# Optimization experiments

Hardware: AMD Instinct MI355X
Metric: run time of the kernel (lower is better)

The kernel has to match this reference:

```python
import jax, jax.numpy as jnp
import numpy as np
from jax import lax

B, C, H, W = 4, 256, 32, 32   # latent: NCHW, C == codebook embed dim
N_CODES = 16384


def setup_inputs() -> dict:
    key = jax.random.key(0)
    k1, k2, k3 = jax.random.split(key, 3)
    latent = jax.random.normal(k1, (B, C, H, W), jnp.float32)
    codebook = jax.random.normal(k2, (N_CODES, C), jnp.float32)
    dec_w = jax.random.normal(k3, (3, C, 3, 3), jnp.float32) * 0.02
    dec_b = jnp.zeros((3,), jnp.float32)
    return {"latent": latent, "codebook": codebook, "dec_w": dec_w, "dec_b": dec_b}


def vector_quantize(x, codebook):
    # x: [B,H,W,D], codebook: [N,D]. Squared-L2 nearest neighbor + gather,
    # straight-through gradient (replace_grad(x_q, x)).
    d = ((x * x).sum(-1, keepdims=True)
         - 2.0 * jnp.einsum('bhwd,nd->bhwn', x, codebook)
         + (codebook * codebook).sum(-1))          # [B,H,W,N]
    idx = jnp.argmin(d, axis=-1)                    # [B,H,W]
    x_q = codebook[idx]                             # gather -> [B,H,W,D]
    return x + lax.stop_gradient(x_q - x)


@jax.custom_vjp
def clamp_with_grad(x):
    return jnp.clip(x, 0.0, 1.0)

def _cwg_fwd(x):
    return jnp.clip(x, 0.0, 1.0), x

def _cwg_bwd(x, g):
    # pass gradient only where it points back toward the valid range
    keep = (g * (x - jnp.clip(x, 0.0, 1.0)) >= 0).astype(g.dtype)
    return (g * keep,)

clamp_with_grad.defvjp(_cwg_fwd, _cwg_bwd)


def decode(quant, dec_w, dec_b):
    # stub VQGAN decoder: single 3x3 conv embed_dim -> 3 (NCHW)
    y = lax.conv_general_dilated(quant, dec_w, window_strides=(1, 1),
                                 padding='SAME',
                                 dimension_numbers=('NCHW', 'OIHW', 'NCHW'))
    return y + dec_b[None, :, None, None]


def reference(latent, codebook, dec_w, dec_b):
    x = jnp.moveaxis(latent, 1, 3)                  # NCHW -> NHWC
    quant = jnp.moveaxis(vector_quantize(x, codebook), 3, 1)  # back to NCHW
    img = decode(quant, dec_w, dec_b)
    return clamp_with_grad((img + 1.0) * 0.5)
```

## Files before the change

### kernel.cpp

```cpp
#include <hip/hip_runtime.h>
#include <hip/hip_bf16.h>
#include <stdint.h>

#define P_TOT   4096
#define N_CODE  16384
#define DIM     256
#define HW      1024
#define CHW     262144
#define NBLK    16

typedef unsigned long long u64;
typedef unsigned short u16;
typedef __attribute__((ext_vector_type(4))) float f32x4;
typedef __attribute__((ext_vector_type(8))) short bf16x8;
typedef __attribute__((ext_vector_type(8))) unsigned short ushort8;

#define FENCE() asm volatile("" ::: "memory")
#define BAR()   __builtin_amdgcn_s_barrier()
#define VM(n)   asm volatile("s_waitcnt vmcnt(" #n ")" ::: "memory")

__device__ __forceinline__ unsigned int mono(float f) {
  unsigned int u = __float_as_uint(f);
  return (u & 0x80000000u) ? ~u : (u | 0x80000000u);
}
__device__ __forceinline__ u16 f2bf(float f) {
  __hip_bfloat16 h = __float2bfloat16(f);
  return *(u16*)&h;
}
__device__ __forceinline__ float bf2f(u16 b) {
  __hip_bfloat16 h = *(__hip_bfloat16*)&b;
  return __bfloat162float(h);
}
__device__ __forceinline__ void gload16(const void* g, void* l) {
  __builtin_amdgcn_global_load_lds(
      (const __attribute__((address_space(1))) unsigned int*)g,
      (__attribute__((address_space(3))) unsigned int*)l, 16, 0, 0);
}

__global__ __launch_bounds__(256) void k_prep(const float* __restrict__ cb,
                                              const float* __restrict__ latent,
                                              const float* __restrict__ dec_w,
                                              u16* __restrict__ bfrag,
                                              u16* __restrict__ xfrag,
                                              float* __restrict__ xt,
                                              float* __restrict__ cnorm,
                                              float* __restrict__ wt) {
  __shared__ float ls[64][68];
  int bid = blockIdx.x;
  int t = threadIdx.x;
  if (bid < 1024) {
    int blk = bid;
    int kp = blk & 3, bq = (blk >> 2) & 3, nb = blk >> 4;
    int code0 = nb * 256 + bq * 64;
    int k0 = kp * 64;
    int lr = t >> 4, lc = (t & 15) * 4;
    #pragma unroll
    for (int pss = 0; pss < 4; ++pss) {
      int row = pss * 16 + lr;
      float4 v = *(const float4*)&cb[(size_t)(code0 + row) * DIM + k0 + lc];
      ls[row][lc] = v.x; ls[row][lc + 1] = v.y; ls[row][lc + 2] = v.z; ls[row][lc + 3] = v.w;
    }
    __syncthreads();
    int row64 = t & 63, g = t >> 6;
    #pragma unroll
    for (int it = 0; it < 4; ++it) {
      int combo = it * 4 + g;
      int kt2 = combo >> 3, s = (combo >> 1) & 3, h = combo & 1;
      int kt = kp * 2 + kt2;
      ushort8 o;
      #pragma unroll
      for (int e = 0; e < 8; ++e) {
        float x = ls[row64][kt2 * 32 + s * 8 + e];
        u16 hi = f2bf(x);
        o[e] = h ? f2bf(x - bf2f(hi)) : hi;
      }
      size_t unitIdx = (size_t)(nb * 8 + kt) * 4 + bq;
      *(ushort8*)&bfrag[unitIdx * 4096 + (size_t)((h * 4 + s) * 64 + row64) * 8] = o;
    }
  } else if (bid < 1280) {
    int blk = bid - 1024;
    int kp = blk & 3, rowblk = blk >> 2;
    int g0 = rowblk * 64;
    int b = g0 >> 10, hw0 = g0 & 1023;
    int c0 = kp * 64;
    int ch = t >> 4, px4 = (t & 15) * 4;
    #pragma unroll
    for (int pss = 0; pss < 4; ++pss) {
      int c = pss * 16 + ch;
      float4 v = *(const float4*)&latent[(size_t)b * CHW + (size_t)(c0 + c) * HW + hw0 + px4];
      ls[px4 + 0][c] = v.x; ls[px4 + 1][c] = v.y; ls[px4 + 2][c] = v.z; ls[px4 + 3][c] = v.w;
    }
    __syncthreads();
    int row64 = t & 63, g = t >> 6;
    #pragma unroll
    for (int it = 0; it < 4; ++it) {
      int combo = it * 4 + g;
      int kt2 = combo >> 3, s = (combo >> 1) & 3, h = combo & 1;
      int kt = kp * 2 + kt2;
      ushort8 o;
      #pragma unroll
      for (int e = 0; e < 8; ++e) {
        float x = ls[row64][kt2 * 32 + s * 8 + e];
        u16 hi = f2bf(x);
        o[e] = h ? f2bf(x - bf2f(hi)) : hi;
      }
      int mbO = rowblk >> 2, aq = rowblk & 3;
      size_t unitIdx = (size_t)(mbO * 8 + kt) * 4 + aq;
      *(ushort8*)&xfrag[unitIdx * 4096 + (size_t)((h * 4 + s) * 64 + row64) * 8] = o;
    }
    int pix = t >> 2, sub = t & 3;
    #pragma unroll
    for (int q = 0; q < 4; ++q) {
      int c = sub * 16 + q * 4;
      float4 v;
      v.x = ls[pix][c]; v.y = ls[pix][c + 1]; v.z = ls[pix][c + 2]; v.w = ls[pix][c + 3];
      *(float4*)&xt[(size_t)(g0 + pix) * DIM + c0 + c] = v;
    }
  } else if (bid < 5376) {
    int code = (bid - 1280) * 4 + (t >> 6);
    int lane = t & 63;
    float4 v = ((const float4*)(cb + (size_t)code * DIM))[lane];
    float sv = fmaf(v.x, v.x, fmaf(v.y, v.y, fmaf(v.z, v.z, v.w * v.w)));
    #pragma unroll
    for (int off = 32; off; off >>= 1) sv += __shfl_down(sv, off, 64);
    if (lane == 0) cnorm[code] = sv;
  } else {
    int e = (bid - 5376) * 256 + t;
    if (e < 6912) {
      int ic = e & 255; int r = e >> 8;
      int kx = r % 3; r /= 3; int ky = r % 3; int oc = r / 3;
      wt[e] = dec_w[((oc * 256 + ic) * 3 + ky) * 3 + kx];
    }
  }
}

__global__ __launch_bounds__(512, 2) void k_vq(const u16* __restrict__ xfrag,
                                               const u16* __restrict__ bfrag,
                                               const float* __restrict__ cnorm,
                                               u64* __restrict__ partial) {
  __shared__ u16 lds[2][2][4][4096];
  __shared__ float cnl[1024];
  __shared__ u64 red[256][4];

  int bid = blockIdx.x;
  int xcd = bid & 7, ix = bid >> 3;
  int nbc = xcd * 2 + (ix >> 4);
  int mb  = ix & 15;

  int tid = threadIdx.x, lane = tid & 63, w = tid >> 6;
  int fr = lane & 15, s = lane >> 4;
  int wr = w >> 2, wc = w & 3;
  int tid8 = tid * 8;

  const u16* Xb = xfrag + (size_t)mb * 32 * 4096;
  const u16* Bb = bfrag + (size_t)nbc * 128 * 4096;

  cnl[tid]       = cnorm[nbc * 1024 + tid];
  cnl[tid + 512] = cnorm[nbc * 1024 + 512 + tid];
  ((u64*)red)[tid]       = ~0ull;
  ((u64*)red)[tid + 512] = ~0ull;
  __syncthreads();

  #pragma unroll
  for (int r = 0; r < 4; ++r) gload16(Xb + (size_t)r * 4096 + tid8, &lds[0][0][r][0] + tid8);
  #pragma unroll
  for (int r = 0; r < 4; ++r) gload16(Bb + (size_t)r * 4096 + tid8, &lds[0][1][r][0] + tid8);
  VM(0); BAR(); FENCE();

  f32x4 acc[8][4] = {};

  #define FOLD(pp) {                                                          \
    float cnv[4]; unsigned codev[4];                                          \
    _Pragma("unroll")                                                         \
    for (int nf = 0; nf < 4; ++nf) {                                          \
      cnv[nf] = cnl[(pp) * 256 + wc * 64 + nf * 16 + fr];                     \
      codev[nf] = (unsigned)(nbc * 1024 + (pp) * 256 + wc * 64 + nf * 16 + fr); \
    }                                                                         \
    _Pragma("unroll")                                                         \
    for (int mfr = 0; mfr < 8; ++mfr) {                                       \
      u64 bb[4];                                                              \
      _Pragma("unroll")                                                       \
      for (int rr = 0; rr < 4; ++rr) {                                        \
        u64 m = ~0ull;                                                        \
        _Pragma("unroll")                                                     \
        for (int nf = 0; nf < 4; ++nf) {                                      \
          float val = fmaf(-2.0f, acc[mfr][nf][rr], cnv[nf]);                 \
          u64 key = ((u64)mono(val) << 32) | codev[nf];                       \
          if (key < m) m = key;                                               \
        }                                                                     \
        bb[rr] = m;                                                           \
      }                                                                       \
      _Pragma("unroll")                                                       \
      for (int d = 1; d < 16; d <<= 1) {                                      \
        _Pragma("unroll")                                                     \
        for (int rr = 0; rr < 4; ++rr) {                                      \
          u64 o = __shfl_xor(bb[rr], d, 64);                                  \
          if (o < bb[rr]) bb[rr] = o;                                         \
        }                                                                     \
      }                                                                       \
      if (fr == 0) {                                                          \
        _Pragma("unroll")                                                     \
        for (int rr = 0; rr < 4; ++rr) {                                      \
          int row = wr * 128 + mfr * 16 + s * 4 + rr;                         \
          u64 old = red[row][wc];                                             \
          red[row][wc] = (bb[rr] < old) ? bb[rr] : old;                       \
        }                                                                     \
      }                                                                       \
      _Pragma("unroll")                                                       \
      for (int nf = 0; nf < 4; ++nf)                                          \
        _Pragma("unroll")                                                     \
        for (int rr = 0; rr < 4; ++rr) acc[mfr][nf][rr] = 0.0f;               \
    }                                                                         \
  }

  #pragma unroll 1
  for (int tt = 0; tt < 32; ++tt) {
    const int cur = tt & 1, nxt = cur ^ 1;
    const int kt = tt & 7;
    const u16* LA = &lds[cur][0][0][0];
    const u16* LB = &lds[cur][1][0][0];
    if (tt < 31) {
      const u16* SA = Xb + (size_t)((tt + 1) & 7) * 16384;
      const u16* SB = Bb + (size_t)(tt + 1) * 16384;
      #pragma unroll
      for (int r = 0; r < 4; ++r) gload16(SA + (size_t)r * 4096 + tid8, &lds[nxt][0][r][0] + tid8);
      #pragma unroll
      for (int r = 0; r < 4; ++r) gload16(SB + (size_t)r * 4096 + tid8, &lds[nxt][1][r][0] + tid8);
    }
    bf16x8 bh[4], bl[4];
    #pragma unroll
    for (int nf = 0; nf < 4; ++nf) {
      bh[nf] = *(const bf16x8*)&LB[wc * 4096 + (size_t)((0 + s) * 64 + nf * 16 + fr) * 8];
      bl[nf] = *(const bf16x8*)&LB[wc * 4096 + (size_t)((4 + s) * 64 + nf * 16 + fr) * 8];
    }
    #pragma unroll
    for (int mfr = 0; mfr < 8; ++mfr) {
      const int au = wr * 2 + (mfr >> 2);
      const int r64 = (mfr & 3) * 16 + fr;
      bf16x8 ah = *(const bf16x8*)&LA[au * 4096 + (size_t)((0 + s) * 64 + r64) * 8];
      bf16x8 al = *(const bf16x8*)&LA[au * 4096 + (size_t)((4 + s) * 64 + r64) * 8];
      __builtin_amdgcn_s_setprio(1);
      #pragma unroll
      for (int nf = 0; nf < 4; ++nf)
        acc[mfr][nf] = __builtin_amdgcn_mfma_f32_16x16x32_bf16(ah, bh[nf], acc[mfr][nf], 0, 0, 0);
      #pragma unroll
      for (int nf = 0; nf < 4; ++nf)
        acc[mfr][nf] = __builtin_amdgcn_mfma_f32_16x16x32_bf16(ah, bl[nf], acc[mfr][nf], 0, 0, 0);
      #pragma unroll
      for (int nf = 0; nf < 4; ++nf)
        acc[mfr][nf] = __builtin_amdgcn_mfma_f32_16x16x32_bf16(al, bh[nf], acc[mfr][nf], 0, 0, 0);
      __builtin_amdgcn_s_setprio(0);
    }
    if (kt == 7) { FOLD(tt >> 3); }
    VM(0);
    BAR(); FENCE();
  }

  if (tid < 256) {
    u64 m0 = red[tid][0], m1 = red[tid][1], m2 = red[tid][2], m3 = red[tid][3];
    u64 a = m0 < m1 ? m0 : m1;
    u64 b2 = m2 < m3 ? m2 : m3;
    partial[(size_t)(mb * 256 + tid) * NBLK + nbc] = a < b2 ? a : b2;
  }
}

__global__ __launch_bounds__(256) void k_idx(const u64* __restrict__ partial,
                                             const float* __restrict__ xt,
                                             const float* __restrict__ cb,
                                             int* __restrict__ idxo) {
  int p = (blockIdx.x * 256 + threadIdx.x) >> 6;
  int lane = threadIdx.x & 63;
  u64 v = (lane < NBLK) ? partial[(size_t)p * NBLK + lane] : ~0ull;
  u64 m1 = v;
  #pragma unroll
  for (int d = 1; d < 64; d <<= 1) { u64 o = __shfl_xor(m1, d, 64); if (o < m1) m1 = o; }
  u64 vv = (v == m1) ? ~0ull : v;
  u64 m2 = vv;
  #pragma unroll
  for (int d = 1; d < 64; d <<= 1) { u64 o = __shfl_xor(m2, d, 64); if (o < m2) m2 = o; }
  int n1 = (int)(m1 & 0xFFFFFFFFull);
  int n2 = (int)(m2 & 0xFFFFFFFFull);

  float4 xv = *(const float4*)&xt[(size_t)p * DIM + lane * 4];
  float4 ca = *(const float4*)&cb[(size_t)n1 * DIM + lane * 4];
  float4 cbv = *(const float4*)&cb[(size_t)n2 * DIM + lane * 4];
  double d1, d2;
  {
    double e0 = (double)xv.x - (double)ca.x, e1 = (double)xv.y - (double)ca.y;
    double e2 = (double)xv.z - (double)ca.z, e3 = (double)xv.w - (double)ca.w;
    d1 = e0 * e0 + e1 * e1 + e2 * e2 + e3 * e3;
  }
  {
    double e0 = (double)xv.x - (double)cbv.x, e1 = (double)xv.y - (double)cbv.y;
    double e2 = (double)xv.z - (double)cbv.z, e3 = (double)xv.w - (double)cbv.w;
    d2 = e0 * e0 + e1 * e1 + e2 * e2 + e3 * e3;
  }
  #pragma unroll
  for (int d = 32; d; d >>= 1) {
    d1 += __shfl_down(d1, d, 64);
    d2 += __shfl_down(d2, d, 64);
  }
  if (lane == 0) {
    idxo[p] = (d2 < d1 || (d2 == d1 && n2 < n1)) ? n2 : n1;
  }
}

__global__ __launch_bounds__(256) void k_conv(const int* __restrict__ idxo,
                                              const float* __restrict__ cb,
                                              const float* __restrict__ wt,
                                              const float* __restrict__ bias,
                                              float* __restrict__ out) {
  __shared__ int idxl[3][32];
  int y = blockIdx.x, b = blockIdx.y;
  int t = threadIdx.x;
  if (t < 96) {
    int r = t >> 5, px = t & 31;
    int yy = min(max(y + r - 1, 0), 31);
    idxl[r][px] = idxo[b * HW + yy * 32 + px];
  }
  __syncthreads();

  int x = t & 31, icg = t >> 5;
  float a0 = 0.f, a1 = 0.f, a2 = 0.f;
  #pragma unroll
  for (int dy = -1; dy <= 1; dy++) {
    int yy = y + dy;
    if (yy < 0 || yy >= 32) continue;
    #pragma unroll
    for (int dx = -1; dx <= 1; dx++) {
      int xx = x + dx;
      if (xx < 0 || xx >= 32) continue;
      int n = idxl[dy + 1][xx];
      const float4* crow = (const float4*)(cb + (size_t)n * DIM + icg * 32);
      int tap = (dy + 1) * 3 + (dx + 1);
      const float4* w0p = (const float4*)(wt + (size_t)(0 * 9 + tap) * DIM + icg * 32);
      const float4* w1p = (const float4*)(wt + (size_t)(1 * 9 + tap) * DIM + icg * 32);
      const float4* w2p = (const float4*)(wt + (size_t)(2 * 9 + tap) * DIM + icg * 32);
      #pragma unroll
      for (int q = 0; q < 8; q++) {
        float4 qv = crow[q];
        float4 wa = w0p[q];
        a0 = fmaf(qv.x, wa.x, a0); a0 = fmaf(qv.y, wa.y, a0);
        a0 = fmaf(qv.z, wa.z, a0); a0 = fmaf(qv.w, wa.w, a0);
        float4 wb = w1p[q];
        a1 = fmaf(qv.x, wb.x, a1); a1 = fmaf(qv.y, wb.y, a1);
        a1 = fmaf(qv.z, wb.z, a1); a1 = fmaf(qv.w, wb.w, a1);
        float4 wcv = w2p[q];
        a2 = fmaf(qv.x, wcv.x, a2); a2 = fmaf(qv.y, wcv.y, a2);
        a2 = fmaf(qv.z, wcv.z, a2); a2 = fmaf(qv.w, wcv.w, a2);
      }
    }
  }
  __shared__ float red[3][32][8];
  red[0][x][icg] = a0; red[1][x][icg] = a1; red[2][x][icg] = a2;
  __syncthreads();
  if (t < 96) {
    int oc = t >> 5, xo = t & 31;
    float sum = 0.f;
    #pragma unroll
    for (int k = 0; k < 8; k++) sum += red[oc][xo][k];
    sum += bias[oc];
    sum = (sum + 1.0f) * 0.5f;
    sum = fminf(fmaxf(sum, 0.0f), 1.0f);
    out[((size_t)(b * 3 + oc) * 32 + y) * 32 + xo] = sum;
  }
}

extern "C" void kernel_launch(void* const* d_in, const int* in_sizes, int n_in,
                              void* d_out, int out_size, void* d_ws, size_t ws_size,
                              hipStream_t stream) {
  const float* latent = (const float*)d_in[0];
  const float* cb     = (const float*)d_in[1];
  const float* dec_w  = (const float*)d_in[2];
  const float* dec_b  = (const float*)d_in[3];
  float* out = (float*)d_out;

  char* ws = (char*)d_ws;
  u64*   partial = (u64*)ws;
  float* cnorm   = (float*)(ws + 0x080000);
  int*   idx     = (int*)  (ws + 0x090000);
  float* wt      = (float*)(ws + 0x094000);
  u16*   xfrag   = (u16*)  (ws + 0x100000);
  u16*   bfrag   = (u16*)  (ws + 0x800000);
  float* xt      = (float*)(ws + 0x1800000);

  k_prep<<<dim3(5403), dim3(256), 0, stream>>>(cb, latent, dec_w, bfrag, xfrag, xt, cnorm, wt);
  k_vq  <<<dim3(256),  dim3(512), 0, stream>>>(xfrag, bfrag, cnorm, partial);
  k_idx <<<dim3(1024), dim3(256), 0, stream>>>(partial, xt, cb, idx);
  k_conv<<<dim3(32, 4), dim3(256), 0, stream>>>(idx, cb, wt, dec_b, out);
}
```

Before: 206.4 us.

## Reshape VQ warp tiling to 4x2 and fuse codebook norms into prep

The VQ GEMM warp layout changes from 2x4 to 4x2 waves. Each wave now holds 4 A row-fragments and 8 B column-fragments, with all A fragments loaded before the async prefetch and B read in two halves. The change is meant to cut repeated LDS reads of A per wave and improve MFMA issue density, at the cost of more live registers. Separately, codebook squared norms are now computed inside the bfrag conversion blocks using shuffles plus atomicAdd, after a memset. This removes 4096 extra prep blocks that reread the codebook, but the norms become a float atomic sum whose summation order is nondeterministic.

```diff
diff --git a/kernel.cpp b/kernel.cpp
--- a/kernel.cpp
+++ b/kernel.cpp
@@ -18,6 +18,7 @@
 #define FENCE() asm volatile("" ::: "memory")
 #define BAR()   __builtin_amdgcn_s_barrier()
 #define VM(n)   asm volatile("s_waitcnt vmcnt(" #n ")" ::: "memory")
+#define LGKM0() asm volatile("s_waitcnt lgkmcnt(0)" ::: "memory")
 
 __device__ __forceinline__ unsigned int mono(float f) {
   unsigned int u = __float_as_uint(f);
@@ -59,6 +60,10 @@
       int row = pss * 16 + lr;
       float4 v = *(const float4*)&cb[(size_t)(code0 + row) * DIM + k0 + lc];
       ls[row][lc] = v.x; ls[row][lc + 1] = v.y; ls[row][lc + 2] = v.z; ls[row][lc + 3] = v.w;
+      float nrm = fmaf(v.x, v.x, fmaf(v.y, v.y, fmaf(v.z, v.z, v.w * v.w)));
+      #pragma unroll
+      for (int d = 1; d < 16; d <<= 1) nrm += __shfl_xor(nrm, d, 64);
+      if ((t & 15) == 0) atomicAdd(&cnorm[code0 + row], nrm);
     }
     __syncthreads();
     int row64 = t & 63, g = t >> 6;
@@ -116,16 +121,8 @@
       v.x = ls[pix][c]; v.y = ls[pix][c + 1]; v.z = ls[pix][c + 2]; v.w = ls[pix][c + 3];
       *(float4*)&xt[(size_t)(g0 + pix) * DIM + c0 + c] = v;
     }
-  } else if (bid < 5376) {
-    int code = (bid - 1280) * 4 + (t >> 6);
-    int lane = t & 63;
-    float4 v = ((const float4*)(cb + (size_t)code * DIM))[lane];
-    float sv = fmaf(v.x, v.x, fmaf(v.y, v.y, fmaf(v.z, v.z, v.w * v.w)));
-    #pragma unroll
-    for (int off = 32; off; off >>= 1) sv += __shfl_down(sv, off, 64);
-    if (lane == 0) cnorm[code] = sv;
   } else {
-    int e = (bid - 5376) * 256 + t;
+    int e = (bid - 1280) * 256 + t;
     if (e < 6912) {
       int ic = e & 255; int r = e >> 8;
       int kx = r % 3; r /= 3; int ky = r % 3; int oc = r / 3;
@@ -140,7 +137,7 @@
                                                u64* __restrict__ partial) {
   __shared__ u16 lds[2][2][4][4096];
   __shared__ float cnl[1024];
-  __shared__ u64 red[256][4];
+  __shared__ u64 red[256][2];
 
   int bid = blockIdx.x;
   int xcd = bid & 7, ix = bid >> 3;
@@ -149,7 +146,7 @@
 
   int tid = threadIdx.x, lane = tid & 63, w = tid >> 6;
   int fr = lane & 15, s = lane >> 4;
-  int wr = w >> 2, wc = w & 3;
+  int wr = w >> 1, wc = w & 1;
   int tid8 = tid * 8;
 
   const u16* Xb = xfrag + (size_t)mb * 32 * 4096;
@@ -157,8 +154,7 @@
 
   cnl[tid]       = cnorm[nbc * 1024 + tid];
   cnl[tid + 512] = cnorm[nbc * 1024 + 512 + tid];
-  ((u64*)red)[tid]       = ~0ull;
-  ((u64*)red)[tid + 512] = ~0ull;
+  ((u64*)red)[tid] = ~0ull;
   __syncthreads();
 
   #pragma unroll
@@ -167,23 +163,57 @@
   for (int r = 0; r < 4; ++r) gload16(Bb + (size_t)r * 4096 + tid8, &lds[0][1][r][0] + tid8);
   VM(0); BAR(); FENCE();
 
-  f32x4 acc[8][4] = {};
-
+  f32x4 acc[4][8] = {};
+  bf16x8 ah[4], al[4], bh[4], bl[4];
+
+  #define READ_A(LA)                                                          \
+    _Pragma("unroll")                                                         \
+    for (int mfr = 0; mfr < 4; ++mfr) {                                       \
+      ah[mfr] = *(const bf16x8*)&(LA)[wr * 4096 + (size_t)((0 + s) * 64 + mfr * 16 + fr) * 8]; \
+      al[mfr] = *(const bf16x8*)&(LA)[wr * 4096 + (size_t)((4 + s) * 64 + mfr * 16 + fr) * 8]; \
+    }
+  #define READ_B(LB, hh)                                                      \
+    _Pragma("unroll")                                                         \
+    for (int j = 0; j < 4; ++j) {                                             \
+      bh[j] = *(const bf16x8*)&(LB)[(wc * 2 + (hh)) * 4096 + (size_t)((0 + s) * 64 + j * 16 + fr) * 8]; \
+      bl[j] = *(const bf16x8*)&(LB)[(wc * 2 + (hh)) * 4096 + (size_t)((4 + s) * 64 + j * 16 + fr) * 8]; \
+    }
+  #define MFMAH(hh)                                                           \
+    __builtin_amdgcn_s_setprio(1);                                            \
+    _Pragma("unroll")                                                         \
+    for (int mfr = 0; mfr < 4; ++mfr) {                                       \
+      _Pragma("unroll")                                                       \
+      for (int j = 0; j < 4; ++j)                                             \
+        acc[mfr][(hh) * 4 + j] = __builtin_amdgcn_mfma_f32_16x16x32_bf16(ah[mfr], bh[j], acc[mfr][(hh) * 4 + j], 0, 0, 0); \
+    }                                                                         \
+    _Pragma("unroll")                                                         \
+    for (int mfr = 0; mfr < 4; ++mfr) {                                       \
+      _Pragma("unroll")                                                       \
+      for (int j = 0; j < 4; ++j)                                             \
+        acc[mfr][(hh) * 4 + j] = __builtin_amdgcn_mfma_f32_16x16x32_bf16(ah[mfr], bl[j], acc[mfr][(hh) * 4 + j], 0, 0, 0); \
+    }                                                                         \
+    _Pragma("unroll")                                                         \
+    for (int mfr = 0; mfr < 4; ++mfr) {                                       \
+      _Pragma("unroll")                                                       \
+      for (int j = 0; j < 4; ++j)                                             \
+        acc[mfr][(hh) * 4 + j] = __builtin_amdgcn_mfma_f32_16x16x32_bf16(al[mfr], bh[j], acc[mfr][(hh) * 4 + j], 0, 0, 0); \
+    }                                                                         \
+    __builtin_amdgcn_s_setprio(0);
   #define FOLD(pp) {                                                          \
-    float cnv[4]; unsigned codev[4];                                          \
-    _Pragma("unroll")                                                         \
-    for (int nf = 0; nf < 4; ++nf) {                                          \
-      cnv[nf] = cnl[(pp) * 256 + wc * 64 + nf * 16 + fr];                     \
-      codev[nf] = (unsigned)(nbc * 1024 + (pp) * 256 + wc * 64 + nf * 16 + fr); \
+    float cnv[8]; unsigned codev[8];                                          \
+    _Pragma("unroll")                                                         \
+    for (int nf = 0; nf < 8; ++nf) {                                          \
+      cnv[nf] = cnl[(pp) * 256 + wc * 128 + nf * 16 + fr];                    \
+      codev[nf] = (unsigned)(nbc * 1024 + (pp) * 256 + wc * 128 + nf * 16 + fr); \
     }                                                                         \
     _Pragma("unroll")                                                         \
-    for (int mfr = 0; mfr < 8; ++mfr) {                                       \
+    for (int mfr = 0; mfr < 4; ++mfr) {                                       \
       u64 bb[4];                                                              \
       _Pragma("unroll")                                                       \
       for (int rr = 0; rr < 4; ++rr) {                                        \
         u64 m = ~0ull;                                                        \
         _Pragma("unroll")                                                     \
-        for (int nf = 0; nf < 4; ++nf) {                                      \
+        for (int nf = 0; nf < 8; ++nf) {                                      \
           float val = fmaf(-2.0f, acc[mfr][nf][rr], cnv[nf]);                 \
           u64 key = ((u64)mono(val) << 32) | codev[nf];                       \
           if (key < m) m = key;                                               \
@@ -201,13 +231,13 @@
       if (fr == 0) {                                                          \
         _Pragma("unroll")                                                     \
         for (int rr = 0; rr < 4; ++rr) {                                      \
-          int row = wr * 128 + mfr * 16 + s * 4 + rr;                         \
+          int row = wr * 64 + mfr * 16 + s * 4 + rr;                          \
           u64 old = red[row][wc];                                             \
           red[row][wc] = (bb[rr] < old) ? bb[rr] : old;                       \
         }                                                                     \
       }                                                                       \
       _Pragma("unroll")                                                       \
-      for (int nf = 0; nf < 4; ++nf)                                          \
+      for (int nf = 0; nf < 8; ++nf)                                          \
         _Pragma("unroll")                                                     \
         for (int rr = 0; rr < 4; ++rr) acc[mfr][nf][rr] = 0.0f;               \
     }                                                                         \
@@ -219,6 +249,7 @@
     const int kt = tt & 7;
     const u16* LA = &lds[cur][0][0][0];
     const u16* LB = &lds[cur][1][0][0];
+    READ_A(LA); READ_B(LB, 0);
     if (tt < 31) {
       const u16* SA = Xb + (size_t)((tt + 1) & 7) * 16384;
       const u16* SB = Bb + (size_t)(tt + 1) * 16384;
@@ -227,39 +258,16 @@
       #pragma unroll
       for (int r = 0; r < 4; ++r) gload16(SB + (size_t)r * 4096 + tid8, &lds[nxt][1][r][0] + tid8);
     }
-    bf16x8 bh[4], bl[4];
-    #pragma unroll
-    for (int nf = 0; nf < 4; ++nf) {
-      bh[nf] = *(const bf16x8*)&LB[wc * 4096 + (size_t)((0 + s) * 64 + nf * 16 + fr) * 8];
-      bl[nf] = *(const bf16x8*)&LB[wc * 4096 + (size_t)((4 + s) * 64 + nf * 16 + fr) * 8];
-    }
-    #pragma unroll
-    for (int mfr = 0; mfr < 8; ++mfr) {
-      const int au = wr * 2 + (mfr >> 2);
-      const int r64 = (mfr & 3) * 16 + fr;
-      bf16x8 ah = *(const bf16x8*)&LA[au * 4096 + (size_t)((0 + s) * 64 + r64) * 8];
-      bf16x8 al = *(const bf16x8*)&LA[au * 4096 + (size_t)((4 + s) * 64 + r64) * 8];
-      __builtin_amdgcn_s_setprio(1);
-      #pragma unroll
-      for (int nf = 0; nf < 4; ++nf)
-        acc[mfr][nf] = __builtin_amdgcn_mfma_f32_16x16x32_bf16(ah, bh[nf], acc[mfr][nf], 0, 0, 0);
-      #pragma unroll
-      for (int nf = 0; nf < 4; ++nf)
-        acc[mfr][nf] = __builtin_amdgcn_mfma_f32_16x16x32_bf16(ah, bl[nf], acc[mfr][nf], 0, 0, 0);
-      #pragma unroll
-      for (int nf = 0; nf < 4; ++nf)
-        acc[mfr][nf] = __builtin_amdgcn_mfma_f32_16x16x32_bf16(al, bh[nf], acc[mfr][nf], 0, 0, 0);
-      __builtin_amdgcn_s_setprio(0);
-    }
-    if (kt == 7) { FOLD(tt >> 3); }
+    MFMAH(0);
+    READ_B(LB, 1);
+    MFMAH(1);
+    if (kt == 7) { FOLD(tt >> 3); LGKM0(); }
     VM(0);
     BAR(); FENCE();
   }
 
   if (tid < 256) {
-    u64 m0 = red[tid][0], m1 = red[tid][1], m2 = red[tid][2], m3 = red[tid][3];
-    u64 a = m0 < m1 ? m0 : m1;
-    u64 b2 = m2 < m3 ? m2 : m3;
+    u64 a = red[tid][0], b2 = red[tid][1];
     partial[(size_t)(mb * 256 + tid) * NBLK + nbc] = a < b2 ? a : b2;
   }
 }
@@ -384,7 +392,8 @@
   u16*   bfrag   = (u16*)  (ws + 0x800000);
   float* xt      = (float*)(ws + 0x1800000);
 
-  k_prep<<<dim3(5403), dim3(256), 0, stream>>>(cb, latent, dec_w, bfrag, xfrag, xt, cnorm, wt);
+  hipMemsetAsync(cnorm, 0, N_CODE * sizeof(float), stream);
+  k_prep<<<dim3(1307), dim3(256), 0, stream>>>(cb, latent, dec_w, bfrag, xfrag, xt, cnorm, wt);
   k_vq  <<<dim3(256),  dim3(512), 0, stream>>>(xfrag, bfrag, cnorm, partial);
   k_idx <<<dim3(1024), dim3(256), 0, stream>>>(partial, xt, cb, idx);
   k_conv<<<dim3(32, 4), dim3(256), 0, stream>>>(idx, cb, wt, dec_b, out);
```

Result: faster. 186.6 us (-9.6%).
